# Performance work log

Measured on AMD Instinct MI355X. Metric: run time of the kernel, lower is better.

## Reference

```python
import jax, jax.numpy as jnp
import numpy as np

N = 2_000_000   # active sparse points
C = 64          # channels
NUM_INS = 64    # number of instance segments
EPS = 1e-5      # InstanceNorm1d eps


def setup_inputs() -> dict:
    key = jax.random.key(0)
    k1, k2, k3 = jax.random.split(key, 3)
    features = jax.random.normal(k1, (N, C), dtype=jnp.float32)
    ins_indices_batch = jax.random.randint(k2, (N,), 0, NUM_INS).astype(jnp.int32)
    eca_weight = jax.random.normal(k3, (1, 1, 3), dtype=jnp.float32) * 0.1
    return {"features": features, "ins_indices_batch": ins_indices_batch,
            "eca_weight": eca_weight}


def reference(features, ins_indices_batch, eca_weight):
    seg = ins_indices_batch
    ones = jnp.ones((features.shape[0],), features.dtype)
    cnt = jax.ops.segment_sum(ones, seg, num_segments=NUM_INS)[:, None]  # [I,1]
    cnt = jnp.maximum(cnt, 1.0)

    # --- SparseInsGNBNIN (InstanceNorm1d per instance, per channel, biased var) ---
    s = jax.ops.segment_sum(features, seg, num_segments=NUM_INS)              # [I,C]
    s2 = jax.ops.segment_sum(features * features, seg, num_segments=NUM_INS)  # [I,C]
    mu = s / cnt
    var = s2 / cnt - mu * mu
    xn = (features - mu[seg]) * jax.lax.rsqrt(var[seg] + EPS)

    # --- SparseReLU ---
    xr = jax.nn.relu(xn)

    # --- SparseInsECA: per-instance channel mean -> conv1d(k=3) -> sigmoid -> scale ---
    m = jax.ops.segment_sum(xr, seg, num_segments=NUM_INS) / cnt  # [I,C]
    conv = jax.lax.conv_general_dilated(
        m[:, None, :], eca_weight, window_strides=(1,), padding=[(1, 1)],
        dimension_numbers=("NCH", "OIH", "NCH"))[:, 0, :]          # [I,C]
    w = jax.nn.sigmoid(conv)
    return xr * w[seg]
```

## Files before the change

### kernel.cpp

```cpp
#include <hip/hip_runtime.h>

#define NI 64
#define CH 64
#define EPSV 1e-5f
#define KB 32
#define PADT 66
#define PADW 65


__global__ __launch_bounds__(256) void k_hist(const int* __restrict__ seg,
                                              unsigned* __restrict__ hist, int n) {
  __shared__ unsigned h[NI];
  const int t = threadIdx.x;
  if (t < NI) h[t] = 0u;
  __syncthreads();
  const int stride = gridDim.x * 256;
  const int n4 = n >> 2;
  for (int i = blockIdx.x * 256 + t; i < n4; i += stride) {
    const int4 s = reinterpret_cast<const int4*>(seg)[i];
    atomicAdd(&h[s.x], 1u); atomicAdd(&h[s.y], 1u);
    atomicAdd(&h[s.z], 1u); atomicAdd(&h[s.w], 1u);
  }
  if (blockIdx.x == 0)
    for (int i = (n4 << 2) + t; i < n; i += 256) atomicAdd(&h[seg[i]], 1u);
  __syncthreads();
  if (t < NI) atomicAdd(&hist[t], h[t]);
}

__global__ void k_scan(const unsigned* __restrict__ hist,
                       unsigned* __restrict__ off, unsigned* __restrict__ cur) {
  if (threadIdx.x == 0) {
    unsigned acc = 0;
    for (int i = 0; i < NI; ++i) { off[i] = acc; cur[i] = acc; acc += hist[i]; }
    off[NI] = acc;
  }
}

__global__ __launch_bounds__(256) void k_scatter(const int* __restrict__ seg,
                                                 unsigned* __restrict__ g_cur,
                                                 unsigned* __restrict__ perm, int n) {
  __shared__ int stash[8192];
  __shared__ unsigned h[NI];
  __shared__ unsigned base[NI];
  const int t = threadIdx.x;
  const int start = blockIdx.x * 8192;
  const int len = min(8192, n - start);
  if (t < NI) h[t] = 0u;
  __syncthreads();
  for (int i = t; i < len; i += 256) {
    const int s = seg[start + i];
    stash[i] = s;
    atomicAdd(&h[s], 1u);
  }
  __syncthreads();
  if (t < NI) { base[t] = atomicAdd(&g_cur[t], h[t]); h[t] = 0u; }
  __syncthreads();
  for (int i = t; i < len; i += 256) {
    const int s = stash[i];
    const unsigned r = atomicAdd(&h[s], 1u);
    perm[base[s] + r] = (unsigned)(start + i);
  }
}

__global__ __launch_bounds__(256) void k_stats_b(const float* __restrict__ f,
                                                 const unsigned* __restrict__ perm,
                                                 const unsigned* __restrict__ off,
                                                 float* __restrict__ g_s,
                                                 float* __restrict__ g_s2) {
  __shared__ float red[4][128];
  const int ins = blockIdx.x >> 5;
  const int k = blockIdx.x & (KB - 1);
  const unsigned lo = off[ins], len = off[ins + 1] - lo;
  const unsigned a = lo + ((len * (unsigned)k) >> 5);
  const unsigned b = lo + ((len * (unsigned)(k + 1)) >> 5);
  const int t = threadIdx.x;
  const int lane = t & 63;
  const int wv = t >> 6;
  const int psub = lane >> 4;
  const int c0 = (lane & 15) << 2;
  float4 s = {0.f, 0.f, 0.f, 0.f}, s2 = {0.f, 0.f, 0.f, 0.f};
  for (unsigned i = a + (unsigned)(wv * 4 + psub); i < b; i += 16) {
    const unsigned p = perm[i];
    const float4 v = *reinterpret_cast<const float4*>(f + (size_t)p * CH + c0);
    s.x += v.x; s.y += v.y; s.z += v.z; s.w += v.w;
    s2.x = fmaf(v.x, v.x, s2.x); s2.y = fmaf(v.y, v.y, s2.y);
    s2.z = fmaf(v.z, v.z, s2.z); s2.w = fmaf(v.w, v.w, s2.w);
  }
  s.x += __shfl_xor(s.x, 16); s.y += __shfl_xor(s.y, 16);
  s.z += __shfl_xor(s.z, 16); s.w += __shfl_xor(s.w, 16);
  s.x += __shfl_xor(s.x, 32); s.y += __shfl_xor(s.y, 32);
  s.z += __shfl_xor(s.z, 32); s.w += __shfl_xor(s.w, 32);
  s2.x += __shfl_xor(s2.x, 16); s2.y += __shfl_xor(s2.y, 16);
  s2.z += __shfl_xor(s2.z, 16); s2.w += __shfl_xor(s2.w, 16);
  s2.x += __shfl_xor(s2.x, 32); s2.y += __shfl_xor(s2.y, 32);
  s2.z += __shfl_xor(s2.z, 32); s2.w += __shfl_xor(s2.w, 32);
  if (psub == 0) {
    *reinterpret_cast<float4*>(&red[wv][c0]) = s;
    *reinterpret_cast<float4*>(&red[wv][64 + c0]) = s2;
  }
  __syncthreads();
  if (t < 128) {
    const float v = red[0][t] + red[1][t] + red[2][t] + red[3][t];
    float* dst = (t < 64) ? (g_s + ins * CH + t) : (g_s2 + ins * CH + (t - 64));
    atomicAdd(dst, v);
  }
}

__global__ __launch_bounds__(256) void k_musig(const float* __restrict__ g_s,
                                               const float* __restrict__ g_s2,
                                               const unsigned* __restrict__ cnt,
                                               float* __restrict__ g_inv,
                                               float* __restrict__ g_mi) {
  const int i = blockIdx.x * 256 + threadIdx.x;
  const float c = fmaxf((float)cnt[i >> 6], 1.f);
  const float mu = g_s[i] / c;
  const float var = fmaxf(g_s2[i] / c - mu * mu, 0.f);
  const float inv = rsqrtf(var + EPSV);
  g_inv[i] = inv;
  g_mi[i] = mu * inv;
}

__global__ __launch_bounds__(256) void k_rsum_b(const float* __restrict__ f,
                                                const unsigned* __restrict__ perm,
                                                const unsigned* __restrict__ off,
                                                const float* __restrict__ g_inv,
                                                const float* __restrict__ g_mi,
                                                float* __restrict__ g_rsum) {
  __shared__ float red[4][64];
  const int ins = blockIdx.x >> 5;
  const int k = blockIdx.x & (KB - 1);
  const unsigned lo = off[ins], len = off[ins + 1] - lo;
  const unsigned a = lo + ((len * (unsigned)k) >> 5);
  const unsigned b = lo + ((len * (unsigned)(k + 1)) >> 5);
  const int t = threadIdx.x;
  const int lane = t & 63;
  const int wv = t >> 6;
  const int psub = lane >> 4;
  const int c0 = (lane & 15) << 2;
  const float4 iv = *reinterpret_cast<const float4*>(g_inv + ins * CH + c0);
  const float4 mi = *reinterpret_cast<const float4*>(g_mi + ins * CH + c0);
  float4 r = {0.f, 0.f, 0.f, 0.f};
  for (unsigned i = a + (unsigned)(wv * 4 + psub); i < b; i += 16) {
    const unsigned p = perm[i];
    const float4 v = *reinterpret_cast<const float4*>(f + (size_t)p * CH + c0);
    r.x += fmaxf(fmaf(v.x, iv.x, -mi.x), 0.f);
    r.y += fmaxf(fmaf(v.y, iv.y, -mi.y), 0.f);
    r.z += fmaxf(fmaf(v.z, iv.z, -mi.z), 0.f);
    r.w += fmaxf(fmaf(v.w, iv.w, -mi.w), 0.f);
  }
  r.x += __shfl_xor(r.x, 16); r.y += __shfl_xor(r.y, 16);
  r.z += __shfl_xor(r.z, 16); r.w += __shfl_xor(r.w, 16);
  r.x += __shfl_xor(r.x, 32); r.y += __shfl_xor(r.y, 32);
  r.z += __shfl_xor(r.z, 32); r.w += __shfl_xor(r.w, 32);
  if (psub == 0) *reinterpret_cast<float4*>(&red[wv][c0]) = r;
  __syncthreads();
  if (t < 64)
    atomicAdd(&g_rsum[ins * CH + t], red[0][t] + red[1][t] + red[2][t] + red[3][t]);
}

__global__ __launch_bounds__(256) void k_eca(const float* __restrict__ g_rsum,
                                             const unsigned* __restrict__ cnt,
                                             const float* __restrict__ ew,
                                             const float* __restrict__ g_inv,
                                             const float* __restrict__ g_mi,
                                             float* __restrict__ g_A,
                                             float* __restrict__ g_B) {
  __shared__ float m[NI * CH];
  const int t = threadIdx.x;
  for (int i = t; i < NI * CH; i += 256)
    m[i] = g_rsum[i] / fmaxf((float)cnt[i >> 6], 1.f);
  __syncthreads();
  const float e0 = ew[0], e1 = ew[1], e2 = ew[2];
  for (int i = t; i < NI * CH; i += 256) {
    const int c = i & 63;
    const float a = c ? m[i - 1] : 0.f;
    const float b = m[i];
    const float d = (c < 63) ? m[i + 1] : 0.f;
    const float conv = e0 * a + e1 * b + e2 * d;
    const float w = 1.f / (1.f + expf(-conv));
    g_A[i] = g_inv[i] * w;
    g_B[i] = g_mi[i] * w;
  }
}

__global__ __launch_bounds__(256) void k_out(const float* __restrict__ f,
                                             const int* __restrict__ seg,
                                             const float* __restrict__ g_A,
                                             const float* __restrict__ g_B,
                                             float* __restrict__ out,
                                             int n) {
  __shared__ float tA[NI * PADT];
  __shared__ float tB[NI * PADT];
  const int t = threadIdx.x;
  for (int i = t; i < NI * CH; i += 256) {
    const int a = (i >> 6) * PADT + (i & 63);
    tA[a] = g_A[i];
    tB[a] = g_B[i];
  }
  __syncthreads();
  const int sub = t & 15;
  const int c0 = sub << 2;
  const int pib = t >> 4;
  const int pstride = gridDim.x << 4;
  for (int p = (blockIdx.x << 4) + pib; p < n; p += pstride) {
    const float4 v = *reinterpret_cast<const float4*>(f + (size_t)p * CH + c0);
    const int tb = seg[p] * PADT + c0;
    const float4 a = *reinterpret_cast<const float4*>(tA + tb);
    const float4 b = *reinterpret_cast<const float4*>(tB + tb);
    float4 o;
    o.x = fmaxf(fmaf(v.x, a.x, -b.x), 0.f);
    o.y = fmaxf(fmaf(v.y, a.y, -b.y), 0.f);
    o.z = fmaxf(fmaf(v.z, a.z, -b.z), 0.f);
    o.w = fmaxf(fmaf(v.w, a.w, -b.w), 0.f);
    *reinterpret_cast<float4*>(out + (size_t)p * CH + c0) = o;
  }
}

__global__ __launch_bounds__(1024) void k_stats_f(const float* __restrict__ f,
                                                  const int* __restrict__ seg,
                                                  float* __restrict__ g_s,
                                                  float* __restrict__ g_s2,
                                                  unsigned* __restrict__ g_cnt, int n) {
  __shared__ float ls[NI * PADW];
  __shared__ float ls2[NI * PADW];
  __shared__ unsigned lcnt[NI];
  const int t = threadIdx.x;
  for (int i = t; i < NI * PADW; i += 1024) { ls[i] = 0.f; ls2[i] = 0.f; }
  if (t < NI) lcnt[t] = 0u;
  __syncthreads();
  const int sub = t & 15, c0 = sub << 2, pib = t >> 4;
  const int pstride = gridDim.x << 6;
  for (int p = (blockIdx.x << 6) + pib; p < n; p += pstride) {
    const float4 v = *reinterpret_cast<const float4*>(f + (size_t)p * CH + c0);
    const int b = seg[p] * PADW + c0;
    atomicAdd(&ls[b + 0], v.x); atomicAdd(&ls[b + 1], v.y);
    atomicAdd(&ls[b + 2], v.z); atomicAdd(&ls[b + 3], v.w);
    atomicAdd(&ls2[b + 0], v.x * v.x); atomicAdd(&ls2[b + 1], v.y * v.y);
    atomicAdd(&ls2[b + 2], v.z * v.z); atomicAdd(&ls2[b + 3], v.w * v.w);
    if (sub == 0) atomicAdd(&lcnt[seg[p]], 1u);
  }
  __syncthreads();
  for (int i = t; i < NI * CH; i += 1024) {
    const int a = (i >> 6) * PADW + (i & 63);
    atomicAdd(&g_s[i], ls[a]);
    atomicAdd(&g_s2[i], ls2[a]);
  }
  if (t < NI) atomicAdd(&g_cnt[t], lcnt[t]);
}

__global__ __launch_bounds__(1024) void k_rsum_f(const float* __restrict__ f,
                                                 const int* __restrict__ seg,
                                                 const float* __restrict__ g_inv,
                                                 const float* __restrict__ g_mi,
                                                 float* __restrict__ g_rsum, int n) {
  __shared__ float tinv[NI * CH];
  __shared__ float tmi[NI * CH];
  __shared__ float lr[NI * PADW];
  const int t = threadIdx.x;
  for (int i = t; i < NI * CH; i += 1024) { tinv[i] = g_inv[i]; tmi[i] = g_mi[i]; }
  for (int i = t; i < NI * PADW; i += 1024) lr[i] = 0.f;
  __syncthreads();
  const int sub = t & 15, c0 = sub << 2, pib = t >> 4;
  const int pstride = gridDim.x << 6;
  for (int p = (blockIdx.x << 6) + pib; p < n; p += pstride) {
    const float4 v = *reinterpret_cast<const float4*>(f + (size_t)p * CH + c0);
    const int ins = seg[p];
    const int tb = (ins << 6) + c0;
    const float4 iv = *reinterpret_cast<const float4*>(tinv + tb);
    const float4 mi = *reinterpret_cast<const float4*>(tmi + tb);
    const int b = ins * PADW + c0;
    atomicAdd(&lr[b + 0], fmaxf(fmaf(v.x, iv.x, -mi.x), 0.f));
    atomicAdd(&lr[b + 1], fmaxf(fmaf(v.y, iv.y, -mi.y), 0.f));
    atomicAdd(&lr[b + 2], fmaxf(fmaf(v.z, iv.z, -mi.z), 0.f));
    atomicAdd(&lr[b + 3], fmaxf(fmaf(v.w, iv.w, -mi.w), 0.f));
  }
  __syncthreads();
  for (int i = t; i < NI * CH; i += 1024)
    atomicAdd(&g_rsum[i], lr[(i >> 6) * PADW + (i & 63)]);
}

extern "C" void kernel_launch(void* const* d_in, const int* in_sizes, int n_in,
                              void* d_out, int out_size, void* d_ws, size_t ws_size,
                              hipStream_t stream) {
  const float* f   = (const float*)d_in[0];
  const int*   seg = (const int*)d_in[1];
  const float* ew  = (const float*)d_in[2];
  float* out = (float*)d_out;
  const int n = in_sizes[1];

  float* ws      = (float*)d_ws;
  float* g_s     = ws;
  float* g_s2    = ws + 4096;
  float* g_rsum  = ws + 8192;
  unsigned* hist = (unsigned*)(ws + 12288);
  unsigned* off  = hist + 64;
  unsigned* cur  = off + 65;
  float* g_inv   = ws + 12544;
  float* g_mi    = ws + 16640;
  float* g_A     = ws + 20736;
  float* g_B     = ws + 24832;
  unsigned* perm = (unsigned*)(ws + 28928);
  const size_t need = (size_t)(28928 + n) * 4;

  hipMemsetAsync(d_ws, 0, (12288 + 64) * sizeof(float), stream);

  if (ws_size >= need) {
    k_hist<<<256, 256, 0, stream>>>(seg, hist, n);
    k_scan<<<1, 64, 0, stream>>>(hist, off, cur);
    k_scatter<<<(n + 8191) / 8192, 256, 0, stream>>>(seg, cur, perm, n);
    k_stats_b<<<NI * KB, 256, 0, stream>>>(f, perm, off, g_s, g_s2);
    k_musig<<<16, 256, 0, stream>>>(g_s, g_s2, hist, g_inv, g_mi);
    k_rsum_b<<<NI * KB, 256, 0, stream>>>(f, perm, off, g_inv, g_mi, g_rsum);
  } else {
    k_stats_f<<<512, 1024, 0, stream>>>(f, seg, g_s, g_s2, hist, n);
    k_musig<<<16, 256, 0, stream>>>(g_s, g_s2, hist, g_inv, g_mi);
    k_rsum_f<<<512, 1024, 0, stream>>>(f, seg, g_inv, g_mi, g_rsum, n);
  }
  k_eca<<<1, 256, 0, stream>>>(g_rsum, hist, ew, g_inv, g_mi, g_A, g_B);
  k_out<<<2048, 256, 0, stream>>>(f, seg, g_A, g_B, out, n);
}
```

Before: 447.0 us.

## Fuse stats, rsum, ECA and output into one persistent kernel with per-instance flags

Replaces the stats, mu/sigma, relu-sum, ECA and output kernels with a single 2048-block kernel. Blocks sync per instance through atomic counters and spin flags: the last block to finish computes the normalisation or ECA weights and the others spin-wait on a flag. This removes four launches and the separate seg-indexed output pass, and the output now runs over the same perm slice each block already touched, which may hit cache. It depends on all 32 blocks of an instance being co-resident (launch_bounds 256,8 is there to help), otherwise the spin-waits can deadlock, and the output writes become scattered by perm order.

```diff
diff --git a/kernel.cpp b/kernel.cpp
--- a/kernel.cpp
+++ b/kernel.cpp
@@ -7,7 +7,6 @@
 #define PADT 66
 #define PADW 65
 
-
 __global__ __launch_bounds__(256) void k_hist(const int* __restrict__ seg,
                                               unsigned* __restrict__ hist, int n) {
   __shared__ unsigned h[NI];
@@ -62,12 +61,23 @@
   }
 }
 
-__global__ __launch_bounds__(256) void k_stats_b(const float* __restrict__ f,
-                                                 const unsigned* __restrict__ perm,
-                                                 const unsigned* __restrict__ off,
-                                                 float* __restrict__ g_s,
-                                                 float* __restrict__ g_s2) {
+__global__ __launch_bounds__(256, 8) void k_fused(
+    const float* __restrict__ f, const unsigned* __restrict__ perm,
+    const unsigned* __restrict__ off, const unsigned* __restrict__ cnt,
+    const float* __restrict__ ew,
+    float* __restrict__ g_s, float* __restrict__ g_s2, float* __restrict__ g_rsum,
+    float* __restrict__ g_inv, float* __restrict__ g_mi,
+    float* __restrict__ g_A, float* __restrict__ g_B,
+    unsigned* __restrict__ ctrl,
+    float* __restrict__ out) {
   __shared__ float red[4][128];
+  __shared__ float liv[CH], lmi[CH], lA[CH], lB[CH], lm[CH];
+  __shared__ int lastf;
+  unsigned* done1 = ctrl;
+  unsigned* flag1 = ctrl + 64;
+  unsigned* done2 = ctrl + 128;
+  unsigned* flag2 = ctrl + 192;
+
   const int ins = blockIdx.x >> 5;
   const int k = blockIdx.x & (KB - 1);
   const unsigned lo = off[ins], len = off[ins + 1] - lo;
@@ -78,31 +88,128 @@
   const int wv = t >> 6;
   const int psub = lane >> 4;
   const int c0 = (lane & 15) << 2;
-  float4 s = {0.f, 0.f, 0.f, 0.f}, s2 = {0.f, 0.f, 0.f, 0.f};
-  for (unsigned i = a + (unsigned)(wv * 4 + psub); i < b; i += 16) {
-    const unsigned p = perm[i];
-    const float4 v = *reinterpret_cast<const float4*>(f + (size_t)p * CH + c0);
-    s.x += v.x; s.y += v.y; s.z += v.z; s.w += v.w;
-    s2.x = fmaf(v.x, v.x, s2.x); s2.y = fmaf(v.y, v.y, s2.y);
-    s2.z = fmaf(v.z, v.z, s2.z); s2.w = fmaf(v.w, v.w, s2.w);
-  }
-  s.x += __shfl_xor(s.x, 16); s.y += __shfl_xor(s.y, 16);
-  s.z += __shfl_xor(s.z, 16); s.w += __shfl_xor(s.w, 16);
-  s.x += __shfl_xor(s.x, 32); s.y += __shfl_xor(s.y, 32);
-  s.z += __shfl_xor(s.z, 32); s.w += __shfl_xor(s.w, 32);
-  s2.x += __shfl_xor(s2.x, 16); s2.y += __shfl_xor(s2.y, 16);
-  s2.z += __shfl_xor(s2.z, 16); s2.w += __shfl_xor(s2.w, 16);
-  s2.x += __shfl_xor(s2.x, 32); s2.y += __shfl_xor(s2.y, 32);
-  s2.z += __shfl_xor(s2.z, 32); s2.w += __shfl_xor(s2.w, 32);
-  if (psub == 0) {
-    *reinterpret_cast<float4*>(&red[wv][c0]) = s;
-    *reinterpret_cast<float4*>(&red[wv][64 + c0]) = s2;
+  const float c = fmaxf((float)cnt[ins], 1.f);
+
+  {
+    float4 s = {0.f, 0.f, 0.f, 0.f}, s2 = {0.f, 0.f, 0.f, 0.f};
+    for (unsigned i = a + (unsigned)(wv * 4 + psub); i < b; i += 16) {
+      const unsigned p = perm[i];
+      const float4 v = *reinterpret_cast<const float4*>(f + (size_t)p * CH + c0);
+      s.x += v.x; s.y += v.y; s.z += v.z; s.w += v.w;
+      s2.x = fmaf(v.x, v.x, s2.x); s2.y = fmaf(v.y, v.y, s2.y);
+      s2.z = fmaf(v.z, v.z, s2.z); s2.w = fmaf(v.w, v.w, s2.w);
+    }
+    s.x += __shfl_xor(s.x, 16); s.y += __shfl_xor(s.y, 16);
+    s.z += __shfl_xor(s.z, 16); s.w += __shfl_xor(s.w, 16);
+    s.x += __shfl_xor(s.x, 32); s.y += __shfl_xor(s.y, 32);
+    s.z += __shfl_xor(s.z, 32); s.w += __shfl_xor(s.w, 32);
+    s2.x += __shfl_xor(s2.x, 16); s2.y += __shfl_xor(s2.y, 16);
+    s2.z += __shfl_xor(s2.z, 16); s2.w += __shfl_xor(s2.w, 16);
+    s2.x += __shfl_xor(s2.x, 32); s2.y += __shfl_xor(s2.y, 32);
+    s2.z += __shfl_xor(s2.z, 32); s2.w += __shfl_xor(s2.w, 32);
+    if (psub == 0) {
+      *reinterpret_cast<float4*>(&red[wv][c0]) = s;
+      *reinterpret_cast<float4*>(&red[wv][64 + c0]) = s2;
+    }
   }
   __syncthreads();
   if (t < 128) {
     const float v = red[0][t] + red[1][t] + red[2][t] + red[3][t];
     float* dst = (t < 64) ? (g_s + ins * CH + t) : (g_s2 + ins * CH + (t - 64));
     atomicAdd(dst, v);
+  }
+  __syncthreads();
+  if (t == 0) lastf = (atomicAdd(&done1[ins], 1u) == KB - 1) ? 1 : 0;
+  __syncthreads();
+  if (lastf) {
+    if (t < CH) {
+      const float st = atomicAdd(&g_s[ins * CH + t], 0.f);
+      const float s2t = atomicAdd(&g_s2[ins * CH + t], 0.f);
+      const float mu = st / c;
+      const float var = fmaxf(s2t / c - mu * mu, 0.f);
+      const float inv = rsqrtf(var + EPSV);
+      liv[t] = inv; lmi[t] = mu * inv;
+      atomicExch(&g_inv[ins * CH + t], inv);
+      atomicExch(&g_mi[ins * CH + t], mu * inv);
+    }
+    __syncthreads();
+    if (t == 0) atomicExch(&flag1[ins], 1u);
+  } else {
+    if (t == 0)
+      while (atomicAdd(&flag1[ins], 0u) == 0u) __builtin_amdgcn_s_sleep(8);
+    __syncthreads();
+    if (t < CH) {
+      liv[t] = atomicAdd(&g_inv[ins * CH + t], 0.f);
+      lmi[t] = atomicAdd(&g_mi[ins * CH + t], 0.f);
+    }
+  }
+  __syncthreads();
+
+  {
+    const float4 iv = *reinterpret_cast<const float4*>(&liv[c0]);
+    const float4 mi = *reinterpret_cast<const float4*>(&lmi[c0]);
+    float4 r = {0.f, 0.f, 0.f, 0.f};
+    for (unsigned i = a + (unsigned)(wv * 4 + psub); i < b; i += 16) {
+      const unsigned p = perm[i];
+      const float4 v = *reinterpret_cast<const float4*>(f + (size_t)p * CH + c0);
+      r.x += fmaxf(fmaf(v.x, iv.x, -mi.x), 0.f);
+      r.y += fmaxf(fmaf(v.y, iv.y, -mi.y), 0.f);
+      r.z += fmaxf(fmaf(v.z, iv.z, -mi.z), 0.f);
+      r.w += fmaxf(fmaf(v.w, iv.w, -mi.w), 0.f);
+    }
+    r.x += __shfl_xor(r.x, 16); r.y += __shfl_xor(r.y, 16);
+    r.z += __shfl_xor(r.z, 16); r.w += __shfl_xor(r.w, 16);
+    r.x += __shfl_xor(r.x, 32); r.y += __shfl_xor(r.y, 32);
+    r.z += __shfl_xor(r.z, 32); r.w += __shfl_xor(r.w, 32);
+    if (psub == 0) *reinterpret_cast<float4*>(&red[wv][c0]) = r;
+  }
+  __syncthreads();
+  if (t < CH)
+    atomicAdd(&g_rsum[ins * CH + t], red[0][t] + red[1][t] + red[2][t] + red[3][t]);
+  __syncthreads();
+  if (t == 0) lastf = (atomicAdd(&done2[ins], 1u) == KB - 1) ? 1 : 0;
+  __syncthreads();
+  if (lastf) {
+    if (t < CH) lm[t] = atomicAdd(&g_rsum[ins * CH + t], 0.f) / c;
+    __syncthreads();
+    if (t < CH) {
+      const float e0 = ew[0], e1 = ew[1], e2 = ew[2];
+      const float ma = t ? lm[t - 1] : 0.f;
+      const float mb = lm[t];
+      const float md = (t < CH - 1) ? lm[t + 1] : 0.f;
+      const float conv = e0 * ma + e1 * mb + e2 * md;
+      const float w = 1.f / (1.f + expf(-conv));
+      const float A = liv[t] * w, B = lmi[t] * w;
+      lA[t] = A; lB[t] = B;
+      atomicExch(&g_A[ins * CH + t], A);
+      atomicExch(&g_B[ins * CH + t], B);
+    }
+    __syncthreads();
+    if (t == 0) atomicExch(&flag2[ins], 1u);
+  } else {
+    if (t == 0)
+      while (atomicAdd(&flag2[ins], 0u) == 0u) __builtin_amdgcn_s_sleep(8);
+    __syncthreads();
+    if (t < CH) {
+      lA[t] = atomicAdd(&g_A[ins * CH + t], 0.f);
+      lB[t] = atomicAdd(&g_B[ins * CH + t], 0.f);
+    }
+  }
+  __syncthreads();
+
+  {
+    const float4 a4 = *reinterpret_cast<const float4*>(&lA[c0]);
+    const float4 b4 = *reinterpret_cast<const float4*>(&lB[c0]);
+    for (unsigned i = a + (unsigned)(wv * 4 + psub); i < b; i += 16) {
+      const unsigned p = perm[i];
+      const float4 v = *reinterpret_cast<const float4*>(f + (size_t)p * CH + c0);
+      float4 o;
+      o.x = fmaxf(fmaf(v.x, a4.x, -b4.x), 0.f);
+      o.y = fmaxf(fmaf(v.y, a4.y, -b4.y), 0.f);
+      o.z = fmaxf(fmaf(v.z, a4.z, -b4.z), 0.f);
+      o.w = fmaxf(fmaf(v.w, a4.w, -b4.w), 0.f);
+      *reinterpret_cast<float4*>(out + (size_t)p * CH + c0) = o;
+    }
   }
 }
 
@@ -120,44 +227,6 @@
   g_mi[i] = mu * inv;
 }
 
-__global__ __launch_bounds__(256) void k_rsum_b(const float* __restrict__ f,
-                                                const unsigned* __restrict__ perm,
-                                                const unsigned* __restrict__ off,
-                                                const float* __restrict__ g_inv,
-                                                const float* __restrict__ g_mi,
-                                                float* __restrict__ g_rsum) {
-  __shared__ float red[4][64];
-  const int ins = blockIdx.x >> 5;
-  const int k = blockIdx.x & (KB - 1);
-  const unsigned lo = off[ins], len = off[ins + 1] - lo;
-  const unsigned a = lo + ((len * (unsigned)k) >> 5);
-  const unsigned b = lo + ((len * (unsigned)(k + 1)) >> 5);
-  const int t = threadIdx.x;
-  const int lane = t & 63;
-  const int wv = t >> 6;
-  const int psub = lane >> 4;
-  const int c0 = (lane & 15) << 2;
-  const float4 iv = *reinterpret_cast<const float4*>(g_inv + ins * CH + c0);
-  const float4 mi = *reinterpret_cast<const float4*>(g_mi + ins * CH + c0);
-  float4 r = {0.f, 0.f, 0.f, 0.f};
-  for (unsigned i = a + (unsigned)(wv * 4 + psub); i < b; i += 16) {
-    const unsigned p = perm[i];
-    const float4 v = *reinterpret_cast<const float4*>(f + (size_t)p * CH + c0);
-    r.x += fmaxf(fmaf(v.x, iv.x, -mi.x), 0.f);
-    r.y += fmaxf(fmaf(v.y, iv.y, -mi.y), 0.f);
-    r.z += fmaxf(fmaf(v.z, iv.z, -mi.z), 0.f);
-    r.w += fmaxf(fmaf(v.w, iv.w, -mi.w), 0.f);
-  }
-  r.x += __shfl_xor(r.x, 16); r.y += __shfl_xor(r.y, 16);
-  r.z += __shfl_xor(r.z, 16); r.w += __shfl_xor(r.w, 16);
-  r.x += __shfl_xor(r.x, 32); r.y += __shfl_xor(r.y, 32);
-  r.z += __shfl_xor(r.z, 32); r.w += __shfl_xor(r.w, 32);
-  if (psub == 0) *reinterpret_cast<float4*>(&red[wv][c0]) = r;
-  __syncthreads();
-  if (t < 64)
-    atomicAdd(&g_rsum[ins * CH + t], red[0][t] + red[1][t] + red[2][t] + red[3][t]);
-}
-
 __global__ __launch_bounds__(256) void k_eca(const float* __restrict__ g_rsum,
                                              const unsigned* __restrict__ cnt,
                                              const float* __restrict__ ew,
@@ -172,10 +241,10 @@
   __syncthreads();
   const float e0 = ew[0], e1 = ew[1], e2 = ew[2];
   for (int i = t; i < NI * CH; i += 256) {
-    const int c = i & 63;
-    const float a = c ? m[i - 1] : 0.f;
+    const int cch = i & 63;
+    const float a = cch ? m[i - 1] : 0.f;
     const float b = m[i];
-    const float d = (c < 63) ? m[i + 1] : 0.f;
+    const float d = (cch < 63) ? m[i + 1] : 0.f;
     const float conv = e0 * a + e1 * b + e2 * d;
     const float w = 1.f / (1.f + expf(-conv));
     g_A[i] = g_inv[i] * w;
@@ -187,8 +256,7 @@
                                              const int* __restrict__ seg,
                                              const float* __restrict__ g_A,
                                              const float* __restrict__ g_B,
-                                             float* __restrict__ out,
-                                             int n) {
+                                             float* __restrict__ out, int n) {
   __shared__ float tA[NI * PADT];
   __shared__ float tB[NI * PADT];
   const int t = threadIdx.x;
@@ -198,9 +266,7 @@
     tB[a] = g_B[i];
   }
   __syncthreads();
-  const int sub = t & 15;
-  const int c0 = sub << 2;
-  const int pib = t >> 4;
+  const int sub = t & 15, c0 = sub << 2, pib = t >> 4;
   const int pstride = gridDim.x << 4;
   for (int p = (blockIdx.x << 4) + pib; p < n; p += pstride) {
     const float4 v = *reinterpret_cast<const float4*>(f + (size_t)p * CH + c0);
@@ -295,27 +361,28 @@
   unsigned* hist = (unsigned*)(ws + 12288);
   unsigned* off  = hist + 64;
   unsigned* cur  = off + 65;
-  float* g_inv   = ws + 12544;
-  float* g_mi    = ws + 16640;
-  float* g_A     = ws + 20736;
-  float* g_B     = ws + 24832;
-  unsigned* perm = (unsigned*)(ws + 28928);
-  const size_t need = (size_t)(28928 + n) * 4;
-
-  hipMemsetAsync(d_ws, 0, (12288 + 64) * sizeof(float), stream);
+  unsigned* ctrl = (unsigned*)(ws + 12544);
+  float* g_inv   = ws + 12800;
+  float* g_mi    = ws + 16896;
+  float* g_A     = ws + 20992;
+  float* g_B     = ws + 25088;
+  unsigned* perm = (unsigned*)(ws + 29184);
+  const size_t need = (size_t)(29184 + n) * 4;
+
+  hipMemsetAsync(d_ws, 0, 12800 * sizeof(float), stream);
 
   if (ws_size >= need) {
     k_hist<<<256, 256, 0, stream>>>(seg, hist, n);
     k_scan<<<1, 64, 0, stream>>>(hist, off, cur);
     k_scatter<<<(n + 8191) / 8192, 256, 0, stream>>>(seg, cur, perm, n);
-    k_stats_b<<<NI * KB, 256, 0, stream>>>(f, perm, off, g_s, g_s2);
-    k_musig<<<16, 256, 0, stream>>>(g_s, g_s2, hist, g_inv, g_mi);
-    k_rsum_b<<<NI * KB, 256, 0, stream>>>(f, perm, off, g_inv, g_mi, g_rsum);
+    k_fused<<<NI * KB, 256, 0, stream>>>(f, perm, off, hist, ew,
+                                         g_s, g_s2, g_rsum, g_inv, g_mi,
+                                         g_A, g_B, ctrl, out);
   } else {
     k_stats_f<<<512, 1024, 0, stream>>>(f, seg, g_s, g_s2, hist, n);
     k_musig<<<16, 256, 0, stream>>>(g_s, g_s2, hist, g_inv, g_mi);
     k_rsum_f<<<512, 1024, 0, stream>>>(f, seg, g_inv, g_mi, g_rsum, n);
-  }
-  k_eca<<<1, 256, 0, stream>>>(g_rsum, hist, ew, g_inv, g_mi, g_A, g_B);
-  k_out<<<2048, 256, 0, stream>>>(f, seg, g_A, g_B, out, n);
-}
+    k_eca<<<1, 256, 0, stream>>>(g_rsum, hist, ew, g_inv, g_mi, g_A, g_B);
+    k_out<<<2048, 256, 0, stream>>>(f, seg, g_A, g_B, out, n);
+  }
+}
```

Result: slower. 467.0 us (+4.5%).
